# Performance work log

Hardware: AMD Instinct MI355X
Metric: run time of the kernel (lower is better)

## Reference

```python
import jax, jax.numpy as jnp
import numpy as np

E = 256
H = 8
B = 131072
N_ATTN = 6  # gd, gc, dg, dc, cg, cd


def setup_inputs() -> dict:
    key = jax.random.key(0)
    ks = jax.random.split(key, 16)
    s = 0.05  # init scale ~ 1/sqrt(E)
    inp = {
        "genomic_embed": jax.random.normal(ks[0], (B, E), jnp.float32),
        "drug_embed": jax.random.normal(ks[1], (B, E), jnp.float32),
        "clinical_embed": jax.random.normal(ks[2], (B, E), jnp.float32),
        # six MultiheadAttention modules, stacked along axis 0
        "Wq": jax.random.normal(ks[3], (N_ATTN, E, E), jnp.float32) * s,
        "Wk": jax.random.normal(ks[4], (N_ATTN, E, E), jnp.float32) * s,
        "Wv": jax.random.normal(ks[5], (N_ATTN, E, E), jnp.float32) * s,
        "bq": jax.random.normal(ks[6], (N_ATTN, E), jnp.float32) * s,
        "bk": jax.random.normal(ks[7], (N_ATTN, E), jnp.float32) * s,
        "bv": jax.random.normal(ks[8], (N_ATTN, E), jnp.float32) * s,
        "Wo": jax.random.normal(ks[9], (N_ATTN, E, E), jnp.float32) * s,
        "bo": jax.random.normal(ks[10], (N_ATTN, E), jnp.float32) * s,
        # fusion MLP: Linear(3E -> 2E), ReLU, Linear(2E -> E)
        "W1": jax.random.normal(ks[11], (2 * E, 3 * E), jnp.float32) * s,
        "b1": jax.random.normal(ks[12], (2 * E,), jnp.float32) * s,
        "W2": jax.random.normal(ks[13], (E, 2 * E), jnp.float32) * s,
        "b2": jax.random.normal(ks[14], (E,), jnp.float32) * s,
    }
    return inp


def _mha1(q_in, kv_in, Wq, Wk, Wv, bq, bk, bv, Wo, bo):
    """MultiheadAttention with seq_len=1 for both query and key/value.
    q_in, kv_in: [B, E]. Returns [B, E]. Dropout is eval-mode identity."""
    D = E // H
    q = (q_in @ Wq.T + bq).reshape(-1, H, D)
    k = (kv_in @ Wk.T + bk).reshape(-1, H, D)
    v = (kv_in @ Wv.T + bv).reshape(-1, H, D)
    # single key: scores [B, H, 1]; softmax over the 1-key axis is identically 1,
    # kept for mathematical faithfulness to the original module
    scores = jnp.sum(q * k, axis=-1, keepdims=True) / jnp.sqrt(jnp.float32(D))
    attn = jax.nn.softmax(scores, axis=-1)
    out = (attn * v).reshape(-1, E)
    return out @ Wo.T + bo


def reference(genomic_embed, drug_embed, clinical_embed,
              Wq, Wk, Wv, bq, bk, bv, Wo, bo, W1, b1, W2, b2):
    g, d, c = genomic_embed, drug_embed, clinical_embed
    # six cross attentions: (query, kv) pairs in module order
    def att(i, q_in, kv_in):
        return _mha1(q_in, kv_in, Wq[i], Wk[i], Wv[i],
                     bq[i], bk[i], bv[i], Wo[i], bo[i])
    gd = att(0, g, d)
    gc = att(1, g, c)
    dg = att(2, d, g)
    dc = att(3, d, c)
    cg = att(4, c, g)
    cd = att(5, c, d)
    g_att = g + gd + gc
    d_att = d + dg + dc
    c_att = c + cg + cd
    combined = jnp.concatenate([g_att, d_att, c_att], axis=-1)  # [B, 3E]
    hidden = jax.nn.relu(combined @ W1.T + b1)                  # [B, 2E]
    fused = hidden @ W2.T + b2                                  # [B, E]
    return fused
```

## Files before the change

kernel.cpp:

```cpp
#include <hip/hip_runtime.h>
#include <cstdint>
#include <cstddef>


typedef __attribute__((ext_vector_type(8))) short short8;
typedef __attribute__((ext_vector_type(4))) float float4v;

__device__ __forceinline__ unsigned short f2bf(float f) {
  union { float f; unsigned u; } v; v.f = f;
  unsigned r = v.u + 0x7FFFu + ((v.u >> 16) & 1u);
  return (unsigned short)(r >> 16);
}

__global__ __launch_bounds__(256) void k_wf(const float* __restrict__ Wo,
                                            const float* __restrict__ Wv,
                                            float* __restrict__ Wf) {
  int b = blockIdx.x;
  int i = b >> 8, m = b & 255;
  int n = threadIdx.x;
  const float* wo = Wo + i * 65536 + m * 256;
  const float* wv = Wv + i * 65536 + n;
  float acc = 0.f;
#pragma unroll 4
  for (int k = 0; k < 256; ++k) acc += wo[k] * wv[k * 256];
  Wf[i * 65536 + m * 256 + n] = acc;
}

__global__ __launch_bounds__(256) void k_bf(const float* __restrict__ Wo,
                                            const float* __restrict__ bv,
                                            const float* __restrict__ bo,
                                            float* __restrict__ bfs) {
  int p = blockIdx.x;
  int m = threadIdx.x;
  int a = 2 * p, b2i = 2 * p + 1;
  float acc = bo[a * 256 + m] + bo[b2i * 256 + m];
  for (int k = 0; k < 256; ++k) {
    acc += Wo[a * 65536 + m * 256 + k] * bv[a * 256 + k];
    acc += Wo[b2i * 65536 + m * 256 + k] * bv[b2i * 256 + k];
  }
  bfs[p * 256 + m] = acc;
}

__global__ __launch_bounds__(256) void k_fold(const float* __restrict__ W1,
                                              const float* __restrict__ Wf,
                                              unsigned short* __restrict__ ATS) {
  int b = blockIdx.x;
  int n = b & 511, p = b >> 9;
  int kk = threadIdx.x;
  int fA, oA, fB, oB;
  if (p == 0)      { fA = 2; oA = 256; fB = 4; oB = 512; }
  else if (p == 1) { fA = 0; oA = 0;   fB = 5; oB = 512; }
  else             { fA = 1; oA = 0;   fB = 3; oB = 256; }
  const float* w1n = W1 + n * 768;
  float val = w1n[p * 256 + kk];
  const float* wfa = Wf + fA * 65536 + kk;
  const float* wfb = Wf + fB * 65536 + kk;
#pragma unroll 4
  for (int j = 0; j < 256; ++j) {
    val += w1n[oA + j] * wfa[j * 256];
    val += w1n[oB + j] * wfb[j * 256];
  }
  int k = p * 256 + kk;
  int t = k >> 5, kq = (k >> 3) & 3, j8 = k & 7;
  int unit = n * 4 + (kq ^ (n & 3));
  ATS[t * 16384 + unit * 8 + j8] = f2bf(val);
}

__global__ __launch_bounds__(256) void k_biash(const float* __restrict__ W1,
                                               const float* __restrict__ b1,
                                               const float* __restrict__ bfs,
                                               float* __restrict__ bias_h) {
  int n = blockIdx.x;
  int kk = threadIdx.x;
  const float* w1n = W1 + n * 768;
  float v = w1n[kk] * bfs[kk] + w1n[256 + kk] * bfs[256 + kk] +
            w1n[512 + kk] * bfs[512 + kk];
  __shared__ float red[256];
  red[kk] = v; __syncthreads();
  for (int s = 128; s > 0; s >>= 1) { if (kk < s) red[kk] += red[kk + s]; __syncthreads(); }
  if (kk == 0) bias_h[n] = red[0] + b1[n];
}

__global__ __launch_bounds__(256) void k_w2(const float* __restrict__ W2,
                                            unsigned short* __restrict__ W2p) {
  int id = blockIdx.x * 256 + threadIdx.x;
  int cpos = id >> 14;
  int n = (id >> 6) & 255;
  int kp = id & 63;
  int t = kp >> 4, ci = kp & 15;
  W2p[id] = f2bf(W2[n * 512 + (cpos + 8 * t) * 16 + ci]);
}

__global__ __launch_bounds__(512, 2) void k_main(
    const float* __restrict__ G, const float* __restrict__ D,
    const float* __restrict__ C, const unsigned short* __restrict__ ATS,
    const float* __restrict__ bias_h, const unsigned short* __restrict__ W2p,
    const float* __restrict__ b2, float* __restrict__ Out) {
  __shared__ unsigned short ats[16384];
  __shared__ unsigned short xt[128][40];
  __shared__ unsigned short hid[128][72];

  const int tid = threadIdx.x;
  const int lane = tid & 63, wave = tid >> 6;
  const int l15 = lane & 15, lq = lane >> 4;
  const int m0 = blockIdx.x * 128;

  const int wm = wave >> 2, wn = wave & 3;

  float4v acc1[4][8];
#pragma unroll
  for (int j = 0; j < 8; ++j) {
    float bh = bias_h[wn * 128 + j * 16 + l15];
#pragma unroll
    for (int i = 0; i < 4; ++i) acc1[i][j] = (float4v){bh, bh, bh, bh};
  }

  const int xrow = tid >> 2, xseg = tid & 3;

  for (int kt = 0; kt < 24; ++kt) {
    const int k0 = kt * 32;
    const float* Xsrc = (k0 < 256) ? G : (k0 < 512) ? D : C;
    const int kc = k0 & 255;

    const float* xp = Xsrc + (size_t)(m0 + xrow) * 256 + kc + xseg * 8;
    float4v f0 = *(const float4v*)xp;
    float4v f1 = *(const float4v*)(xp + 4);
    short8 xv;
    xv[0] = f2bf(f0[0]); xv[1] = f2bf(f0[1]); xv[2] = f2bf(f0[2]); xv[3] = f2bf(f0[3]);
    xv[4] = f2bf(f1[0]); xv[5] = f2bf(f1[1]); xv[6] = f2bf(f1[2]); xv[7] = f2bf(f1[3]);
    *(short8*)&xt[xrow][xseg * 8] = xv;

    const char* gsrc = (const char*)ATS + (size_t)kt * 32768;
#pragma unroll
    for (int it = 0; it < 4; ++it) {
      __builtin_amdgcn_global_load_lds(
          (const __attribute__((address_space(1))) unsigned int*)(gsrc + it * 8192 + tid * 16),
          (__attribute__((address_space(3))) unsigned int*)((char*)ats + it * 8192 + tid * 16),
          16, 0, 0);
    }
    __syncthreads();

    short8 a[4];
#pragma unroll
    for (int i = 0; i < 4; ++i)
      a[i] = *(const short8*)&xt[wm * 64 + i * 16 + l15][lq * 8];
#pragma unroll
    for (int j = 0; j < 8; ++j) {
      int n = wn * 128 + j * 16 + l15;
      int unit = n * 4 + (lq ^ (n & 3));
      short8 bfrag = *(const short8*)&ats[unit * 8];
#pragma unroll
      for (int i = 0; i < 4; ++i)
        acc1[i][j] = __builtin_amdgcn_mfma_f32_16x16x32_bf16(a[i], bfrag, acc1[i][j], 0, 0, 0);
    }
    __syncthreads();
  }

  const int om = wave >> 2, on = wave & 3;
  float4v acc2[4][4];
#pragma unroll
  for (int j = 0; j < 4; ++j) {
    float bb = b2[on * 64 + j * 16 + l15];
#pragma unroll
    for (int i = 0; i < 4; ++i) acc2[i][j] = (float4v){bb, bb, bb, bb};
  }

  for (int cpos = 0; cpos < 8; ++cpos) {
#pragma unroll
    for (int i = 0; i < 4; ++i) {
#pragma unroll
      for (int r = 0; r < 4; ++r) {
        float v = acc1[i][cpos][r];
        v = v > 0.f ? v : 0.f;
        hid[wm * 64 + i * 16 + lq * 4 + r][wn * 16 + l15] = f2bf(v);
      }
    }
    __syncthreads();
#pragma unroll
    for (int ks = 0; ks < 2; ++ks) {
      short8 a2[4];
#pragma unroll
      for (int i = 0; i < 4; ++i)
        a2[i] = *(const short8*)&hid[om * 64 + i * 16 + l15][ks * 32 + lq * 8];
#pragma unroll
      for (int j = 0; j < 4; ++j) {
        int n = on * 64 + j * 16 + l15;
        const unsigned short* bp = W2p + ((size_t)(cpos * 256 + n) * 64 + ks * 32 + lq * 8);
        short8 bfrag = *(const short8*)bp;
#pragma unroll
        for (int i = 0; i < 4; ++i)
          acc2[i][j] = __builtin_amdgcn_mfma_f32_16x16x32_bf16(a2[i], bfrag, acc2[i][j], 0, 0, 0);
      }
    }
    __syncthreads();
  }

#pragma unroll
  for (int i = 0; i < 4; ++i) {
#pragma unroll
    for (int r = 0; r < 4; ++r) {
      int row = m0 + om * 64 + i * 16 + lq * 4 + r;
      float* op = Out + (size_t)row * 256 + on * 64 + l15;
#pragma unroll
      for (int j = 0; j < 4; ++j) op[j * 16] = acc2[i][j][r];
    }
  }
}

extern "C" void kernel_launch(void* const* d_in, const int* in_sizes, int n_in,
                              void* d_out, int out_size, void* d_ws, size_t ws_size,
                              hipStream_t stream) {
  const float* G  = (const float*)d_in[0];
  const float* D  = (const float*)d_in[1];
  const float* C  = (const float*)d_in[2];
  const float* Wv = (const float*)d_in[5];
  const float* bv = (const float*)d_in[8];
  const float* Wo = (const float*)d_in[9];
  const float* bo = (const float*)d_in[10];
  const float* W1 = (const float*)d_in[11];
  const float* b1 = (const float*)d_in[12];
  const float* W2 = (const float*)d_in[13];
  const float* b2 = (const float*)d_in[14];

  char* ws = (char*)d_ws;
  float* Wf           = (float*)(ws);
  float* bfs          = (float*)(ws + 1572864);
  float* bias_h       = (float*)(ws + 1575936);
  unsigned short* ATS = (unsigned short*)(ws + 1577984);
  unsigned short* W2p = (unsigned short*)(ws + 2364416);
  float* Out = (float*)d_out;

  hipLaunchKernelGGL(k_wf,    dim3(1536), dim3(256), 0, stream, Wo, Wv, Wf);
  hipLaunchKernelGGL(k_bf,    dim3(3),    dim3(256), 0, stream, Wo, bv, bo, bfs);
  hipLaunchKernelGGL(k_fold,  dim3(1536), dim3(256), 0, stream, W1, Wf, ATS);
  hipLaunchKernelGGL(k_biash, dim3(512),  dim3(256), 0, stream, W1, b1, bfs, bias_h);
  hipLaunchKernelGGL(k_w2,    dim3(512),  dim3(256), 0, stream, W2, W2p);
  hipLaunchKernelGGL(k_main,  dim3(1024), dim3(512), 0, stream, G, D, C, ATS, bias_h, W2p, b2, Out);
}
```

Measured before the change: 650.2 us.

## Double-buffer main GEMM loads and merge weight-prep kernels into two launches

The main kernel now double-buffers the folded weight tile in LDS and prefetches the next activation tile into registers. It uses manual waitcnt and barrier placement so global loads overlap the MFMA work. The five weight-preparation kernels are merged into two launches, and the k_bf bias fold is parallelised with a shared-memory reduction instead of 3 serial blocks. The inner reductions also use multiple accumulators. This adds 32KB more LDS per block, which may reduce occupancy, and the hand-written vmcnt counts are fragile.

Measured after the change: 584.2 us. 1.11x faster.

```diff
diff --git a/kernel.cpp b/kernel.cpp
--- a/kernel.cpp
+++ b/kernel.cpp
@@ -12,83 +12,91 @@
   return (unsigned short)(r >> 16);
 }
 
-__global__ __launch_bounds__(256) void k_wf(const float* __restrict__ Wo,
-                                            const float* __restrict__ Wv,
-                                            float* __restrict__ Wf) {
+__global__ __launch_bounds__(256) void k_prep1(const float* __restrict__ Wo,
+                                               const float* __restrict__ Wv,
+                                               const float* __restrict__ bv,
+                                               const float* __restrict__ bo,
+                                               float* __restrict__ Wf,
+                                               float* __restrict__ bfs) {
+  __shared__ float red[256];
   int b = blockIdx.x;
-  int i = b >> 8, m = b & 255;
-  int n = threadIdx.x;
-  const float* wo = Wo + i * 65536 + m * 256;
-  const float* wv = Wv + i * 65536 + n;
-  float acc = 0.f;
+  if (b < 1536) {
+    int i = b >> 8, m = b & 255;
+    int n = threadIdx.x;
+    const float* wo = Wo + i * 65536 + m * 256;
+    const float* wv = Wv + i * 65536 + n;
+    float a0 = 0.f, a1 = 0.f, a2 = 0.f, a3 = 0.f;
 #pragma unroll 4
-  for (int k = 0; k < 256; ++k) acc += wo[k] * wv[k * 256];
-  Wf[i * 65536 + m * 256 + n] = acc;
-}
-
-__global__ __launch_bounds__(256) void k_bf(const float* __restrict__ Wo,
-                                            const float* __restrict__ bv,
-                                            const float* __restrict__ bo,
-                                            float* __restrict__ bfs) {
-  int p = blockIdx.x;
-  int m = threadIdx.x;
-  int a = 2 * p, b2i = 2 * p + 1;
-  float acc = bo[a * 256 + m] + bo[b2i * 256 + m];
-  for (int k = 0; k < 256; ++k) {
-    acc += Wo[a * 65536 + m * 256 + k] * bv[a * 256 + k];
-    acc += Wo[b2i * 65536 + m * 256 + k] * bv[b2i * 256 + k];
-  }
-  bfs[p * 256 + m] = acc;
-}
-
-__global__ __launch_bounds__(256) void k_fold(const float* __restrict__ W1,
-                                              const float* __restrict__ Wf,
-                                              unsigned short* __restrict__ ATS) {
+    for (int k = 0; k < 256; k += 4) {
+      a0 += wo[k]     * wv[k * 256];
+      a1 += wo[k + 1] * wv[(k + 1) * 256];
+      a2 += wo[k + 2] * wv[(k + 2) * 256];
+      a3 += wo[k + 3] * wv[(k + 3) * 256];
+    }
+    Wf[i * 65536 + m * 256 + n] = (a0 + a1) + (a2 + a3);
+  } else {
+    int bb = b - 1536;
+    int p = bb >> 8, m = bb & 255;
+    int t = threadIdx.x;
+    int a = 2 * p, b2i = 2 * p + 1;
+    float v = Wo[a * 65536 + m * 256 + t] * bv[a * 256 + t]
+            + Wo[b2i * 65536 + m * 256 + t] * bv[b2i * 256 + t];
+    red[t] = v; __syncthreads();
+    for (int s = 128; s > 0; s >>= 1) { if (t < s) red[t] += red[t + s]; __syncthreads(); }
+    if (t == 0) bfs[p * 256 + m] = red[0] + bo[a * 256 + m] + bo[b2i * 256 + m];
+  }
+}
+
+__global__ __launch_bounds__(256) void k_prep2(const float* __restrict__ W1,
+                                               const float* __restrict__ b1,
+                                               const float* __restrict__ Wf,
+                                               const float* __restrict__ bfs,
+                                               const float* __restrict__ W2,
+                                               unsigned short* __restrict__ ATS,
+                                               float* __restrict__ bias_h,
+                                               unsigned short* __restrict__ W2p) {
+  __shared__ float red[256];
   int b = blockIdx.x;
-  int n = b & 511, p = b >> 9;
-  int kk = threadIdx.x;
-  int fA, oA, fB, oB;
-  if (p == 0)      { fA = 2; oA = 256; fB = 4; oB = 512; }
-  else if (p == 1) { fA = 0; oA = 0;   fB = 5; oB = 512; }
-  else             { fA = 1; oA = 0;   fB = 3; oB = 256; }
-  const float* w1n = W1 + n * 768;
-  float val = w1n[p * 256 + kk];
-  const float* wfa = Wf + fA * 65536 + kk;
-  const float* wfb = Wf + fB * 65536 + kk;
+  if (b < 1536) {
+    int n = b & 511, p = b >> 9;
+    int kk = threadIdx.x;
+    int fA, oA, fB, oB;
+    if (p == 0)      { fA = 2; oA = 256; fB = 4; oB = 512; }
+    else if (p == 1) { fA = 0; oA = 0;   fB = 5; oB = 512; }
+    else             { fA = 1; oA = 0;   fB = 3; oB = 256; }
+    const float* w1n = W1 + n * 768;
+    const float* wfa = Wf + fA * 65536 + kk;
+    const float* wfb = Wf + fB * 65536 + kk;
+    float v0 = w1n[p * 256 + kk], v1 = 0.f, v2 = 0.f, v3 = 0.f;
 #pragma unroll 4
-  for (int j = 0; j < 256; ++j) {
-    val += w1n[oA + j] * wfa[j * 256];
-    val += w1n[oB + j] * wfb[j * 256];
-  }
-  int k = p * 256 + kk;
-  int t = k >> 5, kq = (k >> 3) & 3, j8 = k & 7;
-  int unit = n * 4 + (kq ^ (n & 3));
-  ATS[t * 16384 + unit * 8 + j8] = f2bf(val);
-}
-
-__global__ __launch_bounds__(256) void k_biash(const float* __restrict__ W1,
-                                               const float* __restrict__ b1,
-                                               const float* __restrict__ bfs,
-                                               float* __restrict__ bias_h) {
-  int n = blockIdx.x;
-  int kk = threadIdx.x;
-  const float* w1n = W1 + n * 768;
-  float v = w1n[kk] * bfs[kk] + w1n[256 + kk] * bfs[256 + kk] +
-            w1n[512 + kk] * bfs[512 + kk];
-  __shared__ float red[256];
-  red[kk] = v; __syncthreads();
-  for (int s = 128; s > 0; s >>= 1) { if (kk < s) red[kk] += red[kk + s]; __syncthreads(); }
-  if (kk == 0) bias_h[n] = red[0] + b1[n];
-}
-
-__global__ __launch_bounds__(256) void k_w2(const float* __restrict__ W2,
-                                            unsigned short* __restrict__ W2p) {
-  int id = blockIdx.x * 256 + threadIdx.x;
-  int cpos = id >> 14;
-  int n = (id >> 6) & 255;
-  int kp = id & 63;
-  int t = kp >> 4, ci = kp & 15;
-  W2p[id] = f2bf(W2[n * 512 + (cpos + 8 * t) * 16 + ci]);
+    for (int j = 0; j < 256; j += 2) {
+      v0 += w1n[oA + j]     * wfa[j * 256];
+      v1 += w1n[oA + j + 1] * wfa[(j + 1) * 256];
+      v2 += w1n[oB + j]     * wfb[j * 256];
+      v3 += w1n[oB + j + 1] * wfb[(j + 1) * 256];
+    }
+    float val = (v0 + v1) + (v2 + v3);
+    int k = p * 256 + kk;
+    int t = k >> 5, kq = (k >> 3) & 3, j8 = k & 7;
+    int unit = n * 4 + (kq ^ (n & 3));
+    ATS[t * 16384 + unit * 8 + j8] = f2bf(val);
+  } else if (b < 2048) {
+    int n = b - 1536;
+    int kk = threadIdx.x;
+    const float* w1n = W1 + n * 768;
+    float v = w1n[kk] * bfs[kk] + w1n[256 + kk] * bfs[256 + kk] +
+              w1n[512 + kk] * bfs[512 + kk];
+    red[kk] = v; __syncthreads();
+    for (int s = 128; s > 0; s >>= 1) { if (kk < s) red[kk] += red[kk + s]; __syncthreads(); }
+    if (kk == 0) bias_h[n] = red[0] + b1[n];
+  } else {
+    int id = (b - 2048) * 256 + threadIdx.x;
+    int cpos = id >> 14;
+    int n = (id >> 6) & 255;
+    int kp = id & 63;
+    int t = kp >> 4, ci = kp & 15;
+    W2p[id] = f2bf(W2[n * 512 + (cpos + 8 * t) * 16 + ci]);
+  }
 }
 
 __global__ __launch_bounds__(512, 2) void k_main(
@@ -96,7 +104,7 @@
     const float* __restrict__ C, const unsigned short* __restrict__ ATS,
     const float* __restrict__ bias_h, const unsigned short* __restrict__ W2p,
     const float* __restrict__ b2, float* __restrict__ Out) {
-  __shared__ unsigned short ats[16384];
+  __shared__ unsigned short ats[2][16384];
   __shared__ unsigned short xt[128][40];
   __shared__ unsigned short hid[128][72];
 
@@ -104,7 +112,6 @@
   const int lane = tid & 63, wave = tid >> 6;
   const int l15 = lane & 15, lq = lane >> 4;
   const int m0 = blockIdx.x * 128;
-
   const int wm = wave >> 2, wn = wave & 3;
 
   float4v acc1[4][8];
@@ -116,45 +123,71 @@
   }
 
   const int xrow = tid >> 2, xseg = tid & 3;
-
-  for (int kt = 0; kt < 24; ++kt) {
-    const int k0 = kt * 32;
-    const float* Xsrc = (k0 < 256) ? G : (k0 < 512) ? D : C;
-    const int kc = k0 & 255;
-
-    const float* xp = Xsrc + (size_t)(m0 + xrow) * 256 + kc + xseg * 8;
-    float4v f0 = *(const float4v*)xp;
-    float4v f1 = *(const float4v*)(xp + 4);
-    short8 xv;
-    xv[0] = f2bf(f0[0]); xv[1] = f2bf(f0[1]); xv[2] = f2bf(f0[2]); xv[3] = f2bf(f0[3]);
-    xv[4] = f2bf(f1[0]); xv[5] = f2bf(f1[1]); xv[6] = f2bf(f1[2]); xv[7] = f2bf(f1[3]);
-    *(short8*)&xt[xrow][xseg * 8] = xv;
-
-    const char* gsrc = (const char*)ATS + (size_t)kt * 32768;
-#pragma unroll
-    for (int it = 0; it < 4; ++it) {
-      __builtin_amdgcn_global_load_lds(
-          (const __attribute__((address_space(1))) unsigned int*)(gsrc + it * 8192 + tid * 16),
-          (__attribute__((address_space(3))) unsigned int*)((char*)ats + it * 8192 + tid * 16),
-          16, 0, 0);
-    }
-    __syncthreads();
-
-    short8 a[4];
-#pragma unroll
-    for (int i = 0; i < 4; ++i)
-      a[i] = *(const short8*)&xt[wm * 64 + i * 16 + l15][lq * 8];
-#pragma unroll
-    for (int j = 0; j < 8; ++j) {
-      int n = wn * 128 + j * 16 + l15;
-      int unit = n * 4 + (lq ^ (n & 3));
-      short8 bfrag = *(const short8*)&ats[unit * 8];
-#pragma unroll
-      for (int i = 0; i < 4; ++i)
-        acc1[i][j] = __builtin_amdgcn_mfma_f32_16x16x32_bf16(a[i], bfrag, acc1[i][j], 0, 0, 0);
-    }
-    __syncthreads();
-  }
+  const int xoff = (m0 + xrow) * 256 + xseg * 8;
+
+  float4v f0, f1, g0, g1;
+
+#define ISSUE_X(kt1, ra, rb) do {                                           \
+    int kt_ = (kt1);                                                        \
+    const float* xb_ = (kt_ < 8) ? G : (kt_ < 16) ? D : C;                  \
+    const float* xp_ = xb_ + xoff + (kt_ & 7) * 32;                         \
+    ra = *(const float4v*)xp_;                                              \
+    rb = *(const float4v*)(xp_ + 4);                                        \
+  } while (0)
+
+#define ISSUE_A(kt1, buf) do {                                              \
+    const char* gsrc_ = (const char*)ATS + (size_t)(kt1) * 32768;           \
+    char* ldst_ = (char*)&ats[buf][0];                                      \
+    _Pragma("unroll")                                                       \
+    for (int it_ = 0; it_ < 4; ++it_)                                       \
+      __builtin_amdgcn_global_load_lds(                                     \
+          (const __attribute__((address_space(1))) unsigned int*)(gsrc_ + it_ * 8192 + tid * 16), \
+          (__attribute__((address_space(3))) unsigned int*)(ldst_ + it_ * 8192 + tid * 16), \
+          16, 0, 0);                                                        \
+  } while (0)
+
+#define BODY(kt_, buf, fa, fb, ga, gb, PREF) do {                           \
+    if (PREF) { ISSUE_X((kt_) + 1, ga, gb); ISSUE_A((kt_) + 1, (buf) ^ 1); } \
+    short8 xv_;                                                             \
+    xv_[0] = f2bf(fa[0]); xv_[1] = f2bf(fa[1]);                             \
+    xv_[2] = f2bf(fa[2]); xv_[3] = f2bf(fa[3]);                             \
+    xv_[4] = f2bf(fb[0]); xv_[5] = f2bf(fb[1]);                             \
+    xv_[6] = f2bf(fb[2]); xv_[7] = f2bf(fb[3]);                             \
+    *(short8*)&xt[xrow][xseg * 8] = xv_;                                    \
+    if (PREF) asm volatile("s_waitcnt vmcnt(6) lgkmcnt(0)" ::: "memory");   \
+    else      asm volatile("s_waitcnt vmcnt(0) lgkmcnt(0)" ::: "memory");   \
+    __builtin_amdgcn_s_barrier();                                           \
+    __builtin_amdgcn_sched_barrier(0);                                      \
+    short8 a_[4];                                                           \
+    _Pragma("unroll")                                                       \
+    for (int i_ = 0; i_ < 4; ++i_)                                          \
+      a_[i_] = *(const short8*)&xt[wm * 64 + i_ * 16 + l15][lq * 8];        \
+    _Pragma("unroll")                                                       \
+    for (int j_ = 0; j_ < 8; ++j_) {                                        \
+      int n_ = wn * 128 + j_ * 16 + l15;                                    \
+      int unit_ = n_ * 4 + (lq ^ (n_ & 3));                                 \
+      short8 bf_ = *(const short8*)&ats[buf][unit_ * 8];                    \
+      _Pragma("unroll")                                                     \
+      for (int i_ = 0; i_ < 4; ++i_)                                        \
+        acc1[i_][j_] = __builtin_amdgcn_mfma_f32_16x16x32_bf16(a_[i_], bf_, acc1[i_][j_], 0, 0, 0); \
+    }                                                                       \
+    __builtin_amdgcn_sched_barrier(0);                                      \
+    __builtin_amdgcn_s_barrier();                                           \
+  } while (0)
+
+  ISSUE_X(0, f0, f1);
+  ISSUE_A(0, 0);
+
+  for (int kp = 0; kp < 11; ++kp) {
+    BODY(2 * kp,     0, f0, f1, g0, g1, 1);
+    BODY(2 * kp + 1, 1, g0, g1, f0, f1, 1);
+  }
+  BODY(22, 0, f0, f1, g0, g1, 1);
+  BODY(23, 1, g0, g1, f0, f1, 0);
+
+#undef BODY
+#undef ISSUE_A
+#undef ISSUE_X
 
   const int om = wave >> 2, on = wave & 3;
   float4v acc2[4][4];
@@ -165,6 +198,7 @@
     for (int i = 0; i < 4; ++i) acc2[i][j] = (float4v){bb, bb, bb, bb};
   }
 
+#pragma unroll
   for (int cpos = 0; cpos < 8; ++cpos) {
 #pragma unroll
     for (int i = 0; i < 4; ++i) {
@@ -175,7 +209,9 @@
         hid[wm * 64 + i * 16 + lq * 4 + r][wn * 16 + l15] = f2bf(v);
       }
     }
-    __syncthreads();
+    asm volatile("s_waitcnt lgkmcnt(0)" ::: "memory");
+    __builtin_amdgcn_s_barrier();
+    __builtin_amdgcn_sched_barrier(0);
 #pragma unroll
     for (int ks = 0; ks < 2; ++ks) {
       short8 a2[4];
@@ -192,7 +228,8 @@
           acc2[i][j] = __builtin_amdgcn_mfma_f32_16x16x32_bf16(a2[i], bfrag, acc2[i][j], 0, 0, 0);
       }
     }
-    __syncthreads();
+    __builtin_amdgcn_sched_barrier(0);
+    __builtin_amdgcn_s_barrier();
   }
 
 #pragma unroll
@@ -230,10 +267,7 @@
   unsigned short* W2p = (unsigned short*)(ws + 2364416);
   float* Out = (float*)d_out;
 
-  hipLaunchKernelGGL(k_wf,    dim3(1536), dim3(256), 0, stream, Wo, Wv, Wf);
-  hipLaunchKernelGGL(k_bf,    dim3(3),    dim3(256), 0, stream, Wo, bv, bo, bfs);
-  hipLaunchKernelGGL(k_fold,  dim3(1536), dim3(256), 0, stream, W1, Wf, ATS);
-  hipLaunchKernelGGL(k_biash, dim3(512),  dim3(256), 0, stream, W1, b1, bfs, bias_h);
-  hipLaunchKernelGGL(k_w2,    dim3(512),  dim3(256), 0, stream, W2, W2p);
+  hipLaunchKernelGGL(k_prep1, dim3(2304), dim3(256), 0, stream, Wo, Wv, bv, bo, Wf, bfs);
+  hipLaunchKernelGGL(k_prep2, dim3(2560), dim3(256), 0, stream, W1, b1, Wf, bfs, W2, ATS, bias_h, W2p);
   hipLaunchKernelGGL(k_main,  dim3(1024), dim3(512), 0, stream, G, D, C, ATS, bias_h, W2p, b2, Out);
 }
```
